# Kernel tuning notes

Hardware: AMD Instinct MI355X
Metric: run time of the kernel (lower is better)

## Reference

```python
import jax, jax.numpy as jnp
import numpy as np

N = 100000
F_IN = 128
HID = 128
E = 1600000


def gcn_conv(x, W, b, src, dst, dinv):
    # PyG GCNConv: h = x @ W; out_i = sum_j norm_ij * h_j (incl. self-loop) + b
    h = x @ W  # [N, H]
    norm = dinv[src] * dinv[dst]  # [E]
    msg = h[src] * norm[:, None]  # [E, H]
    agg = jax.ops.segment_sum(msg, dst, num_segments=N)
    agg = agg + h * (dinv * dinv)[:, None]  # self-loop contribution
    return agg + b


def setup_inputs() -> dict:
    key = jax.random.key(0)
    k1, k2, k3, k4, k5 = jax.random.split(key, 5)
    x = jax.random.normal(k1, (N, F_IN), dtype=jnp.float32)
    edge_index = jax.random.randint(k2, (2, E), 0, N, dtype=jnp.int64)
    s = 1.0 / np.sqrt(F_IN)
    W1 = jax.random.normal(k3, (F_IN, HID), dtype=jnp.float32) * s
    b1 = jnp.zeros((HID,), dtype=jnp.float32)
    sh = 1.0 / np.sqrt(HID)
    W2 = jax.random.normal(k4, (HID, HID), dtype=jnp.float32) * sh
    b2 = jnp.zeros((HID,), dtype=jnp.float32)
    Wfc = jax.random.normal(k5, (HID, 2), dtype=jnp.float32) * sh
    bfc = jnp.zeros((2,), dtype=jnp.float32)
    return {"x": x, "edge_index": edge_index, "W1": W1, "b1": b1,
            "W2": W2, "b2": b2, "Wfc": Wfc, "bfc": bfc}


def reference(x, edge_index, W1, b1, W2, b2, Wfc, bfc):
    src, dst = edge_index[0], edge_index[1]
    # degree with self-loops (edge weight 1), computed on target nodes
    deg = jax.ops.segment_sum(jnp.ones((E,), jnp.float32), dst, num_segments=N) + 1.0
    dinv = jax.lax.rsqrt(deg)
    h = jax.nn.relu(gcn_conv(x, W1, b1, src, dst, dinv))
    h = jax.nn.relu(gcn_conv(h, W2, b2, src, dst, dinv))
    logits = h @ Wfc + bfc  # [N, 2]
    return jax.nn.log_softmax(logits, axis=1)
```

## Files before the change

kernel.cpp:

```cpp
#include <hip/hip_runtime.h>
#include <math.h>

#define N_NODES 100000
#define FDIM 128
#define E_EDGES 1600000
#define NSCAN_BLKS ((N_NODES + 1023) / 1024)

typedef unsigned short bf16_t;

__device__ inline bf16_t f2bf(float f) {
    unsigned int u = __float_as_uint(f);
    return (bf16_t)((u + 0x7fffu + ((u >> 16) & 1u)) >> 16);
}
__device__ inline float2 bfpair(unsigned int u) {
    return make_float2(__uint_as_float(u << 16), __uint_as_float(u & 0xffff0000u));
}

__global__ __launch_bounds__(256) void hist_kernel(const int* __restrict__ dst,
                                                   int* __restrict__ cnt) {
    int e = blockIdx.x * blockDim.x + threadIdx.x;
    if (e < E_EDGES) atomicAdd(&cnt[dst[e]], 1);
}

__global__ __launch_bounds__(256) void scan1(const int* __restrict__ cnt,
                                             int* __restrict__ excl,
                                             int* __restrict__ bsum) {
    __shared__ int lds[256];
    const int b = blockIdx.x, t = threadIdx.x;
    const int base = b * 1024 + t * 4;
    int v[4];
#pragma unroll
    for (int q = 0; q < 4; ++q) {
        int i = base + q;
        v[q] = (i < N_NODES) ? cnt[i] : 0;
    }
    int tsum = v[0] + v[1] + v[2] + v[3];
    lds[t] = tsum;
    __syncthreads();
    for (int off = 1; off < 256; off <<= 1) {
        int x = lds[t];
        int y = (t >= off) ? lds[t - off] : 0;
        __syncthreads();
        lds[t] = x + y;
        __syncthreads();
    }
    int texcl = lds[t] - tsum;
    if (t == 255) bsum[b] = lds[t];
    int run = texcl;
#pragma unroll
    for (int q = 0; q < 4; ++q) {
        int i = base + q;
        if (i < N_NODES) excl[i] = run;
        run += v[q];
    }
}

__global__ __launch_bounds__(128) void scan2(int* __restrict__ bsum) {
    __shared__ int lds[128];
    const int t = threadIdx.x;
    int v = (t < NSCAN_BLKS) ? bsum[t] : 0;
    lds[t] = v;
    __syncthreads();
    for (int off = 1; off < 128; off <<= 1) {
        int x = lds[t];
        int y = (t >= off) ? lds[t - off] : 0;
        __syncthreads();
        lds[t] = x + y;
        __syncthreads();
    }
    if (t < NSCAN_BLKS) bsum[t] = lds[t] - v;
}

__global__ __launch_bounds__(256) void scan3(int* __restrict__ rowptr,
                                             const int* __restrict__ bsum,
                                             const int* __restrict__ cnt,
                                             float* __restrict__ dinv) {
    int i = blockIdx.x * blockDim.x + threadIdx.x;
    if (i < N_NODES) {
        rowptr[i] += bsum[i >> 10];
        dinv[i] = rsqrtf((float)cnt[i] + 1.0f);
    }
    if (i == 0) rowptr[N_NODES] = E_EDGES;
}

__global__ __launch_bounds__(256) void scatter_kernel(const int* __restrict__ src,
                                                      const int* __restrict__ dst,
                                                      const int* __restrict__ rowptr,
                                                      int* __restrict__ cursor,
                                                      int* __restrict__ ssrc) {
    int e = blockIdx.x * blockDim.x + threadIdx.x;
    if (e >= E_EDGES) return;
    int d = dst[e];
    int p = rowptr[d] + atomicAdd(&cursor[d], 1);
    ssrc[p] = src[e];
}

#define BM 128
#define TM 8
#define TN 8
__global__ __launch_bounds__(256) void gemm_rt(const float* __restrict__ X,
                                               const float* __restrict__ W,
                                               bf16_t* __restrict__ H) {
    __shared__ float Ws[128 * 128];
    const int tid = threadIdx.x;
    {
        const float4* Wv = (const float4*)W;
        float4* Sv = (float4*)Ws;
#pragma unroll
        for (int i = 0; i < 16; ++i) Sv[i * 256 + tid] = Wv[i * 256 + tid];
    }
    __syncthreads();

    const int tc = (tid & 15) * TN;
    const int tr = (tid >> 4) * TM;
    const long row0 = (long)blockIdx.x * BM + tr;

    const float* xp[TM];
    bool rowok[TM];
#pragma unroll
    for (int r = 0; r < TM; ++r) {
        long rr = row0 + r;
        rowok[r] = (rr < N_NODES);
        xp[r] = X + (rowok[r] ? rr : 0) * 128;
    }

    float acc[TM][TN];
#pragma unroll
    for (int r = 0; r < TM; ++r)
#pragma unroll
        for (int c = 0; c < TN; ++c) acc[r][c] = 0.f;

    float4 xa[TM], xb[TM];
#pragma unroll
    for (int r = 0; r < TM; ++r) xa[r] = ((const float4*)xp[r])[0];

    for (int k4 = 0; k4 < 32; k4 += 2) {
#pragma unroll
        for (int r = 0; r < TM; ++r) xb[r] = ((const float4*)xp[r])[k4 + 1];
#pragma unroll
        for (int kk = 0; kk < 4; ++kk) {
            const int k = k4 * 4 + kk;
            const float4 b0 = *((const float4*)(Ws + k * 128 + tc));
            const float4 b1 = *((const float4*)(Ws + k * 128 + tc + 4));
#pragma unroll
            for (int r = 0; r < TM; ++r) {
                const float xs = ((const float*)&xa[r])[kk];
                acc[r][0] = fmaf(xs, b0.x, acc[r][0]);
                acc[r][1] = fmaf(xs, b0.y, acc[r][1]);
                acc[r][2] = fmaf(xs, b0.z, acc[r][2]);
                acc[r][3] = fmaf(xs, b0.w, acc[r][3]);
                acc[r][4] = fmaf(xs, b1.x, acc[r][4]);
                acc[r][5] = fmaf(xs, b1.y, acc[r][5]);
                acc[r][6] = fmaf(xs, b1.z, acc[r][6]);
                acc[r][7] = fmaf(xs, b1.w, acc[r][7]);
            }
        }
        if (k4 + 2 < 32) {
#pragma unroll
            for (int r = 0; r < TM; ++r) xa[r] = ((const float4*)xp[r])[k4 + 2];
        }
#pragma unroll
        for (int kk = 0; kk < 4; ++kk) {
            const int k = (k4 + 1) * 4 + kk;
            const float4 b0 = *((const float4*)(Ws + k * 128 + tc));
            const float4 b1 = *((const float4*)(Ws + k * 128 + tc + 4));
#pragma unroll
            for (int r = 0; r < TM; ++r) {
                const float xs = ((const float*)&xb[r])[kk];
                acc[r][0] = fmaf(xs, b0.x, acc[r][0]);
                acc[r][1] = fmaf(xs, b0.y, acc[r][1]);
                acc[r][2] = fmaf(xs, b0.z, acc[r][2]);
                acc[r][3] = fmaf(xs, b0.w, acc[r][3]);
                acc[r][4] = fmaf(xs, b1.x, acc[r][4]);
                acc[r][5] = fmaf(xs, b1.y, acc[r][5]);
                acc[r][6] = fmaf(xs, b1.z, acc[r][6]);
                acc[r][7] = fmaf(xs, b1.w, acc[r][7]);
            }
        }
    }

#pragma unroll
    for (int r = 0; r < TM; ++r) {
        if (rowok[r]) {
            uint4 o;
            o.x = (unsigned)f2bf(acc[r][0]) | ((unsigned)f2bf(acc[r][1]) << 16);
            o.y = (unsigned)f2bf(acc[r][2]) | ((unsigned)f2bf(acc[r][3]) << 16);
            o.z = (unsigned)f2bf(acc[r][4]) | ((unsigned)f2bf(acc[r][5]) << 16);
            o.w = (unsigned)f2bf(acc[r][6]) | ((unsigned)f2bf(acc[r][7]) << 16);
            *((uint4*)(H + (size_t)(row0 + r) * 128 + tc)) = o;
        }
    }
}

__global__ __launch_bounds__(256) void agg_kernel(const int* __restrict__ rowptr,
                                                  const int* __restrict__ ssrc,
                                                  const float* __restrict__ dinv,
                                                  const bf16_t* __restrict__ h,
                                                  const float* __restrict__ bias,
                                                  float* __restrict__ out) {
    int gid = blockIdx.x * blockDim.x + threadIdx.x;
    int node = gid >> 6;
    int lane = gid & 63;
    if (node >= N_NODES) return;
    float dd = dinv[node];
    float2 v = bfpair(((const unsigned*)(h + (size_t)node * 128))[lane]);
    float sc = dd * dd;
    float accx = v.x * sc, accy = v.y * sc;
    int j = rowptr[node];
    const int end = rowptr[node + 1];
    for (; j + 3 < end; j += 4) {
        int s0 = ssrc[j], s1 = ssrc[j + 1], s2 = ssrc[j + 2], s3 = ssrc[j + 3];
        float n0 = dinv[s0] * dd, n1 = dinv[s1] * dd;
        float n2 = dinv[s2] * dd, n3 = dinv[s3] * dd;
        float2 v0 = bfpair(((const unsigned*)(h + (size_t)s0 * 128))[lane]);
        float2 v1 = bfpair(((const unsigned*)(h + (size_t)s1 * 128))[lane]);
        float2 v2 = bfpair(((const unsigned*)(h + (size_t)s2 * 128))[lane]);
        float2 v3 = bfpair(((const unsigned*)(h + (size_t)s3 * 128))[lane]);
        accx += v0.x * n0 + v1.x * n1 + v2.x * n2 + v3.x * n3;
        accy += v0.y * n0 + v1.y * n1 + v2.y * n2 + v3.y * n3;
    }
    for (; j < end; ++j) {
        int s0 = ssrc[j];
        float n0 = dinv[s0] * dd;
        float2 v0 = bfpair(((const unsigned*)(h + (size_t)s0 * 128))[lane]);
        accx += v0.x * n0;
        accy += v0.y * n0;
    }
    float2 b = ((const float2*)bias)[lane];
    accx = fmaxf(accx + b.x, 0.f);
    accy = fmaxf(accy + b.y, 0.f);
    ((float2*)(out + (size_t)node * 128))[lane] = make_float2(accx, accy);
}

__global__ __launch_bounds__(256) void agg_fc_kernel(const int* __restrict__ rowptr,
                                                     const int* __restrict__ ssrc,
                                                     const float* __restrict__ dinv,
                                                     const bf16_t* __restrict__ h,
                                                     const float* __restrict__ bias,
                                                     const float* __restrict__ Wfc,
                                                     const float* __restrict__ bfc,
                                                     float* __restrict__ out) {
    int gid = blockIdx.x * blockDim.x + threadIdx.x;
    int node = gid >> 6;
    int lane = gid & 63;
    if (node >= N_NODES) return;
    float dd = dinv[node];
    float2 v = bfpair(((const unsigned*)(h + (size_t)node * 128))[lane]);
    float sc = dd * dd;
    float accx = v.x * sc, accy = v.y * sc;
    int j = rowptr[node];
    const int end = rowptr[node + 1];
    for (; j + 3 < end; j += 4) {
        int s0 = ssrc[j], s1 = ssrc[j + 1], s2 = ssrc[j + 2], s3 = ssrc[j + 3];
        float n0 = dinv[s0] * dd, n1 = dinv[s1] * dd;
        float n2 = dinv[s2] * dd, n3 = dinv[s3] * dd;
        float2 v0 = bfpair(((const unsigned*)(h + (size_t)s0 * 128))[lane]);
        float2 v1 = bfpair(((const unsigned*)(h + (size_t)s1 * 128))[lane]);
        float2 v2 = bfpair(((const unsigned*)(h + (size_t)s2 * 128))[lane]);
        float2 v3 = bfpair(((const unsigned*)(h + (size_t)s3 * 128))[lane]);
        accx += v0.x * n0 + v1.x * n1 + v2.x * n2 + v3.x * n3;
        accy += v0.y * n0 + v1.y * n1 + v2.y * n2 + v3.y * n3;
    }
    for (; j < end; ++j) {
        int s0 = ssrc[j];
        float n0 = dinv[s0] * dd;
        float2 v0 = bfpair(((const unsigned*)(h + (size_t)s0 * 128))[lane]);
        accx += v0.x * n0;
        accy += v0.y * n0;
    }
    float2 b = ((const float2*)bias)[lane];
    accx = fmaxf(accx + b.x, 0.f);
    accy = fmaxf(accy + b.y, 0.f);
    int k0 = lane * 2;
    float a0 = accx * Wfc[k0 * 2 + 0] + accy * Wfc[(k0 + 1) * 2 + 0];
    float a1 = accx * Wfc[k0 * 2 + 1] + accy * Wfc[(k0 + 1) * 2 + 1];
#pragma unroll
    for (int off = 32; off > 0; off >>= 1) {
        a0 += __shfl_down(a0, off);
        a1 += __shfl_down(a1, off);
    }
    if (lane == 0) {
        float l0 = a0 + bfc[0];
        float l1 = a1 + bfc[1];
        float m = fmaxf(l0, l1);
        float lse = m + logf(expf(l0 - m) + expf(l1 - m));
        out[(size_t)node * 2 + 0] = l0 - lse;
        out[(size_t)node * 2 + 1] = l1 - lse;
    }
}

extern "C" void kernel_launch(void* const* d_in, const int* in_sizes, int n_in,
                              void* d_out, int out_size, void* d_ws, size_t ws_size,
                              hipStream_t stream) {
    const float* x   = (const float*)d_in[0];
    const int*   ei  = (const int*)d_in[1];
    const float* W1  = (const float*)d_in[2];
    const float* b1  = (const float*)d_in[3];
    const float* W2  = (const float*)d_in[4];
    const float* b2  = (const float*)d_in[5];
    const float* Wfc = (const float*)d_in[6];
    const float* bfc = (const float*)d_in[7];
    float* out = (float*)d_out;

    const int* src = ei;
    const int* dst = ei + E_EDGES;

    char* wp = (char*)d_ws;
    auto carve = [&](size_t bytes) -> char* {
        char* p = wp;
        wp += (bytes + 255) & ~(size_t)255;
        return p;
    };
    int*    cnt    = (int*)carve(N_NODES * 4);
    int*    rowptr = (int*)carve((N_NODES + 1) * 4);
    int*    cursor = (int*)carve(N_NODES * 4);
    int*    bsum   = (int*)carve(128 * 4);
    int*    ssrc   = (int*)carve((size_t)E_EDGES * 4);
    float*  dinv   = (float*)carve(N_NODES * 4);
    bf16_t* hbuf   = (bf16_t*)carve((size_t)N_NODES * FDIM * 2);
    float*  x2buf  = (float*)carve((size_t)N_NODES * FDIM * 4);

    const int NE_BLK = (E_EDGES + 255) / 256;
    const int NN_BLK = (N_NODES + 255) / 256;
    const int NODE_WAVE_BLK = (N_NODES * 64 + 255) / 256;
    const int GEMM_BLK = (N_NODES + BM - 1) / BM;

    hipMemsetAsync(cnt, 0, N_NODES * sizeof(int), stream);
    hipMemsetAsync(cursor, 0, N_NODES * sizeof(int), stream);
    hist_kernel<<<NE_BLK, 256, 0, stream>>>(dst, cnt);
    scan1<<<NSCAN_BLKS, 256, 0, stream>>>(cnt, rowptr, bsum);
    scan2<<<1, 128, 0, stream>>>(bsum);
    scan3<<<NN_BLK, 256, 0, stream>>>(rowptr, bsum, cnt, dinv);
    scatter_kernel<<<NE_BLK, 256, 0, stream>>>(src, dst, rowptr, cursor, ssrc);

    gemm_rt<<<GEMM_BLK, 256, 0, stream>>>(x, W1, hbuf);
    agg_kernel<<<NODE_WAVE_BLK, 256, 0, stream>>>(rowptr, ssrc, dinv, hbuf, b1, x2buf);

    gemm_rt<<<GEMM_BLK, 256, 0, stream>>>(x2buf, W2, hbuf);
    agg_fc_kernel<<<NODE_WAVE_BLK, 256, 0, stream>>>(rowptr, ssrc, dinv, hbuf, b2,
                                                     Wfc, bfc, out);
}
```

Baseline: 536.8 us.

## Use bf16 MFMA GEMMs, bf16 intermediate activations, and node-partitioned edge passes

The FP32 register-tiled GEMM is replaced by a bf16 MFMA 16x16x32 kernel. Weights are pre-transposed and converted to bf16 by a small kernel, and the layer-1 output is now stored as bf16 to halve its traffic. The histogram and scatter kernels now run 8 passes over the edges, each handling only destinations in one node range, so atomics stay local to a cache-friendly region. This trades lower GEMM precision and 8x redundant reads of dst for less atomic contention, and the MFMA output stores are strided 2-byte writes.

```diff
diff --git a/kernel.cpp b/kernel.cpp
--- a/kernel.cpp
+++ b/kernel.cpp
@@ -5,8 +5,12 @@
 #define FDIM 128
 #define E_EDGES 1600000
 #define NSCAN_BLKS ((N_NODES + 1023) / 1024)
+#define NPASS 8
+#define PASS_NODES 12500
 
 typedef unsigned short bf16_t;
+typedef __attribute__((ext_vector_type(8))) short short8;
+typedef __attribute__((ext_vector_type(4))) float f32x4;
 
 __device__ inline bf16_t f2bf(float f) {
     unsigned int u = __float_as_uint(f);
@@ -18,8 +22,12 @@
 
 __global__ __launch_bounds__(256) void hist_kernel(const int* __restrict__ dst,
                                                    int* __restrict__ cnt) {
-    int e = blockIdx.x * blockDim.x + threadIdx.x;
-    if (e < E_EDGES) atomicAdd(&cnt[dst[e]], 1);
+    int pass = blockIdx.x & (NPASS - 1);
+    int e = (blockIdx.x >> 3) * 256 + threadIdx.x;
+    if (e >= E_EDGES) return;
+    int d = dst[e];
+    if ((unsigned)(d - pass * PASS_NODES) < (unsigned)PASS_NODES)
+        atomicAdd(&cnt[d], 1);
 }
 
 __global__ __launch_bounds__(256) void scan1(const int* __restrict__ cnt,
@@ -88,106 +96,69 @@
                                                       const int* __restrict__ rowptr,
                                                       int* __restrict__ cursor,
                                                       int* __restrict__ ssrc) {
-    int e = blockIdx.x * blockDim.x + threadIdx.x;
+    int pass = blockIdx.x & (NPASS - 1);
+    int e = (blockIdx.x >> 3) * 256 + threadIdx.x;
     if (e >= E_EDGES) return;
     int d = dst[e];
-    int p = rowptr[d] + atomicAdd(&cursor[d], 1);
-    ssrc[p] = src[e];
-}
-
-#define BM 128
-#define TM 8
-#define TN 8
-__global__ __launch_bounds__(256) void gemm_rt(const float* __restrict__ X,
-                                               const float* __restrict__ W,
-                                               bf16_t* __restrict__ H) {
-    __shared__ float Ws[128 * 128];
+    if ((unsigned)(d - pass * PASS_NODES) < (unsigned)PASS_NODES) {
+        int p = rowptr[d] + atomicAdd(&cursor[d], 1);
+        ssrc[p] = src[e];
+    }
+}
+
+__global__ __launch_bounds__(256) void wcvt_kernel(const float* __restrict__ W,
+                                                   bf16_t* __restrict__ Wt) {
+    int idx = blockIdx.x * 256 + threadIdx.x;
+    int k = idx >> 7, c = idx & 127;
+    Wt[c * 128 + k] = f2bf(W[idx]);
+}
+
+template <bool A_IS_F32>
+__global__ __launch_bounds__(256) void gemm_mfma(const void* __restrict__ Aptr,
+                                                 const bf16_t* __restrict__ Wt,
+                                                 bf16_t* __restrict__ H) {
     const int tid = threadIdx.x;
-    {
-        const float4* Wv = (const float4*)W;
-        float4* Sv = (float4*)Ws;
-#pragma unroll
-        for (int i = 0; i < 16; ++i) Sv[i * 256 + tid] = Wv[i * 256 + tid];
-    }
-    __syncthreads();
-
-    const int tc = (tid & 15) * TN;
-    const int tr = (tid >> 4) * TM;
-    const long row0 = (long)blockIdx.x * BM + tr;
-
-    const float* xp[TM];
-    bool rowok[TM];
-#pragma unroll
-    for (int r = 0; r < TM; ++r) {
-        long rr = row0 + r;
-        rowok[r] = (rr < N_NODES);
-        xp[r] = X + (rowok[r] ? rr : 0) * 128;
-    }
-
-    float acc[TM][TN];
-#pragma unroll
-    for (int r = 0; r < TM; ++r)
-#pragma unroll
-        for (int c = 0; c < TN; ++c) acc[r][c] = 0.f;
-
-    float4 xa[TM], xb[TM];
-#pragma unroll
-    for (int r = 0; r < TM; ++r) xa[r] = ((const float4*)xp[r])[0];
-
-    for (int k4 = 0; k4 < 32; k4 += 2) {
-#pragma unroll
-        for (int r = 0; r < TM; ++r) xb[r] = ((const float4*)xp[r])[k4 + 1];
-#pragma unroll
-        for (int kk = 0; kk < 4; ++kk) {
-            const int k = k4 * 4 + kk;
-            const float4 b0 = *((const float4*)(Ws + k * 128 + tc));
-            const float4 b1 = *((const float4*)(Ws + k * 128 + tc + 4));
-#pragma unroll
-            for (int r = 0; r < TM; ++r) {
-                const float xs = ((const float*)&xa[r])[kk];
-                acc[r][0] = fmaf(xs, b0.x, acc[r][0]);
-                acc[r][1] = fmaf(xs, b0.y, acc[r][1]);
-                acc[r][2] = fmaf(xs, b0.z, acc[r][2]);
-                acc[r][3] = fmaf(xs, b0.w, acc[r][3]);
-                acc[r][4] = fmaf(xs, b1.x, acc[r][4]);
-                acc[r][5] = fmaf(xs, b1.y, acc[r][5]);
-                acc[r][6] = fmaf(xs, b1.z, acc[r][6]);
-                acc[r][7] = fmaf(xs, b1.w, acc[r][7]);
-            }
+    const int wave = tid >> 6;
+    const int l = tid & 63;
+    const int r = l & 15;
+    const int g = l >> 4;
+    const int row0 = (blockIdx.x * 4 + wave) * 16;
+    const int arow = min(row0 + r, N_NODES - 1);
+
+    f32x4 acc[8];
+#pragma unroll
+    for (int ct = 0; ct < 8; ++ct) acc[ct] = (f32x4){0.f, 0.f, 0.f, 0.f};
+
+#pragma unroll
+    for (int ks = 0; ks < 4; ++ks) {
+        const int kbase = ks * 32 + g * 8;
+        short8 a;
+        if constexpr (A_IS_F32) {
+            const float* X = (const float*)Aptr;
+            const float4 x0 = *((const float4*)(X + (size_t)arow * 128 + kbase));
+            const float4 x1 = *((const float4*)(X + (size_t)arow * 128 + kbase + 4));
+            a[0] = (short)f2bf(x0.x); a[1] = (short)f2bf(x0.y);
+            a[2] = (short)f2bf(x0.z); a[3] = (short)f2bf(x0.w);
+            a[4] = (short)f2bf(x1.x); a[5] = (short)f2bf(x1.y);
+            a[6] = (short)f2bf(x1.z); a[7] = (short)f2bf(x1.w);
+        } else {
+            const bf16_t* X = (const bf16_t*)Aptr;
+            a = *((const short8*)(X + (size_t)arow * 128 + kbase));
         }
-        if (k4 + 2 < 32) {
-#pragma unroll
-            for (int r = 0; r < TM; ++r) xa[r] = ((const float4*)xp[r])[k4 + 2];
+#pragma unroll
+        for (int ct = 0; ct < 8; ++ct) {
+            short8 b = *((const short8*)(Wt + (ct * 16 + r) * 128 + kbase));
+            acc[ct] = __builtin_amdgcn_mfma_f32_16x16x32_bf16(a, b, acc[ct], 0, 0, 0);
         }
-#pragma unroll
-        for (int kk = 0; kk < 4; ++kk) {
-            const int k = (k4 + 1) * 4 + kk;
-            const float4 b0 = *((const float4*)(Ws + k * 128 + tc));
-            const float4 b1 = *((const float4*)(Ws + k * 128 + tc + 4));
-#pragma unroll
-            for (int r = 0; r < TM; ++r) {
-                const float xs = ((const float*)&xb[r])[kk];
-                acc[r][0] = fmaf(xs, b0.x, acc[r][0]);
-                acc[r][1] = fmaf(xs, b0.y, acc[r][1]);
-                acc[r][2] = fmaf(xs, b0.z, acc[r][2]);
-                acc[r][3] = fmaf(xs, b0.w, acc[r][3]);
-                acc[r][4] = fmaf(xs, b1.x, acc[r][4]);
-                acc[r][5] = fmaf(xs, b1.y, acc[r][5]);
-                acc[r][6] = fmaf(xs, b1.z, acc[r][6]);
-                acc[r][7] = fmaf(xs, b1.w, acc[r][7]);
-            }
-        }
-    }
-
-#pragma unroll
-    for (int r = 0; r < TM; ++r) {
-        if (rowok[r]) {
-            uint4 o;
-            o.x = (unsigned)f2bf(acc[r][0]) | ((unsigned)f2bf(acc[r][1]) << 16);
-            o.y = (unsigned)f2bf(acc[r][2]) | ((unsigned)f2bf(acc[r][3]) << 16);
-            o.z = (unsigned)f2bf(acc[r][4]) | ((unsigned)f2bf(acc[r][5]) << 16);
-            o.w = (unsigned)f2bf(acc[r][6]) | ((unsigned)f2bf(acc[r][7]) << 16);
-            *((uint4*)(H + (size_t)(row0 + r) * 128 + tc)) = o;
+    }
+
+#pragma unroll
+    for (int j = 0; j < 4; ++j) {
+        const int row = row0 + g * 4 + j;
+        if (row < N_NODES) {
+            bf16_t* hp = H + (size_t)row * 128 + r;
+#pragma unroll
+            for (int ct = 0; ct < 8; ++ct) hp[ct * 16] = f2bf(acc[ct][j]);
         }
     }
 }
@@ -197,7 +168,7 @@
                                                   const float* __restrict__ dinv,
                                                   const bf16_t* __restrict__ h,
                                                   const float* __restrict__ bias,
-                                                  float* __restrict__ out) {
+                                                  bf16_t* __restrict__ out) {
     int gid = blockIdx.x * blockDim.x + threadIdx.x;
     int node = gid >> 6;
     int lane = gid & 63;
@@ -229,7 +200,8 @@
     float2 b = ((const float2*)bias)[lane];
     accx = fmaxf(accx + b.x, 0.f);
     accy = fmaxf(accy + b.y, 0.f);
-    ((float2*)(out + (size_t)node * 128))[lane] = make_float2(accx, accy);
+    unsigned o = (unsigned)f2bf(accx) | ((unsigned)f2bf(accy) << 16);
+    ((unsigned*)(out + (size_t)node * 128))[lane] = o;
 }
 
 __global__ __launch_bounds__(256) void agg_fc_kernel(const int* __restrict__ rowptr,
@@ -318,25 +290,30 @@
     int*    ssrc   = (int*)carve((size_t)E_EDGES * 4);
     float*  dinv   = (float*)carve(N_NODES * 4);
     bf16_t* hbuf   = (bf16_t*)carve((size_t)N_NODES * FDIM * 2);
-    float*  x2buf  = (float*)carve((size_t)N_NODES * FDIM * 4);
-
-    const int NE_BLK = (E_EDGES + 255) / 256;
+    bf16_t* x2buf  = (bf16_t*)carve((size_t)N_NODES * FDIM * 2);
+    bf16_t* Wt1    = (bf16_t*)carve(128 * 128 * 2);
+    bf16_t* Wt2    = (bf16_t*)carve(128 * 128 * 2);
+
     const int NN_BLK = (N_NODES + 255) / 256;
     const int NODE_WAVE_BLK = (N_NODES * 64 + 255) / 256;
-    const int GEMM_BLK = (N_NODES + BM - 1) / BM;
+    const int EDGE_PASS_BLK = ((E_EDGES + 255) / 256) * NPASS;
+    const int GEMM_BLK = (N_NODES + 63) / 64;
 
     hipMemsetAsync(cnt, 0, N_NODES * sizeof(int), stream);
     hipMemsetAsync(cursor, 0, N_NODES * sizeof(int), stream);
-    hist_kernel<<<NE_BLK, 256, 0, stream>>>(dst, cnt);
+    hist_kernel<<<EDGE_PASS_BLK, 256, 0, stream>>>(dst, cnt);
     scan1<<<NSCAN_BLKS, 256, 0, stream>>>(cnt, rowptr, bsum);
     scan2<<<1, 128, 0, stream>>>(bsum);
     scan3<<<NN_BLK, 256, 0, stream>>>(rowptr, bsum, cnt, dinv);
-    scatter_kernel<<<NE_BLK, 256, 0, stream>>>(src, dst, rowptr, cursor, ssrc);
-
-    gemm_rt<<<GEMM_BLK, 256, 0, stream>>>(x, W1, hbuf);
+    scatter_kernel<<<EDGE_PASS_BLK, 256, 0, stream>>>(src, dst, rowptr, cursor, ssrc);
+
+    wcvt_kernel<<<64, 256, 0, stream>>>(W1, Wt1);
+    wcvt_kernel<<<64, 256, 0, stream>>>(W2, Wt2);
+
+    gemm_mfma<true><<<GEMM_BLK, 256, 0, stream>>>(x, Wt1, hbuf);
     agg_kernel<<<NODE_WAVE_BLK, 256, 0, stream>>>(rowptr, ssrc, dinv, hbuf, b1, x2buf);
 
-    gemm_rt<<<GEMM_BLK, 256, 0, stream>>>(x2buf, W2, hbuf);
+    gemm_mfma<false><<<GEMM_BLK, 256, 0, stream>>>(x2buf, Wt2, hbuf);
     agg_fc_kernel<<<NODE_WAVE_BLK, 256, 0, stream>>>(rowptr, ssrc, dinv, hbuf, b2,
                                                      Wfc, bfc, out);
 }
```

Result: faster. 461.9 us (-14.0%).
